# Performance work log

Measured on AMD Instinct MI355X. Metric: run time of the kernel, lower is better.

The kernel has to match this reference:

```python
import jax, jax.numpy as jnp
import numpy as np

N = 50000      # nodes
E = 800000     # edges (avg degree 16)
IN = 128       # input feature dim
HID = 32       # per-head hidden dim
H = 4          # attention heads
C = 40         # num classes
SLOPE = 0.2    # leaky relu negative slope


def setup_inputs() -> dict:
    key = jax.random.key(0)
    ks = jax.random.split(key, 14)
    s = 0.05
    inputs = jax.random.normal(ks[0], (N, IN), jnp.float32)
    target = jax.random.normal(ks[1], (N, IN), jnp.float32)
    lamb = jax.random.uniform(ks[2], (1,), jnp.float32)
    src = jax.random.randint(ks[3], (E,), 0, N, jnp.int32)
    dst = jax.random.randint(ks[4], (E,), 0, N, jnp.int32)
    W0 = jax.random.normal(ks[5], (IN, H * HID), jnp.float32) * s
    al0 = jax.random.normal(ks[6], (H, HID), jnp.float32) * s
    ar0 = jax.random.normal(ks[7], (H, HID), jnp.float32) * s
    W1 = jax.random.normal(ks[8], (H * HID, H * HID), jnp.float32) * s
    al1 = jax.random.normal(ks[9], (H, HID), jnp.float32) * s
    ar1 = jax.random.normal(ks[10], (H, HID), jnp.float32) * s
    Wout = jax.random.normal(ks[11], (H * HID, C), jnp.float32) * s
    bout = jnp.zeros((C,), jnp.float32)
    return dict(inputs=inputs, target=target, lamb=lamb,
                W0=W0, al0=al0, ar0=ar0, W1=W1, al1=al1, ar1=ar1,
                Wout=Wout, bout=bout, src=src, dst=dst)


def gat_conv(h, W, al, ar, src, dst, residual):
    # h: [N, in_dim]; W: [in_dim, H*HID]; al/ar: [H, HID]
    feat = (h @ W).reshape(N, H, HID)                  # [N,H,D]
    el = jnp.einsum('nhd,hd->nh', feat, al)            # [N,H]
    er = jnp.einsum('nhd,hd->nh', feat, ar)            # [N,H]
    e = jax.nn.leaky_relu(el[src] + er[dst], SLOPE)    # [E,H]
    # edge softmax over incoming edges of each dst node
    emax = jax.ops.segment_max(e, dst, num_segments=N)  # [N,H]
    ee = jnp.exp(e - emax[dst])                          # [E,H]
    denom = jax.ops.segment_sum(ee, dst, num_segments=N)
    a = ee / denom[dst]                                  # [E,H]
    msg = feat[src] * a[:, :, None]                      # [E,H,D]
    out = jax.ops.segment_sum(msg, dst, num_segments=N)  # [N,H,D]
    if residual:
        out = out + h.reshape(N, H, HID)  # identity residual (in == H*HID)
    return jax.nn.elu(out)


def reference(inputs, target, lamb, W0, al0, ar0, W1, al1, ar1, Wout, bout, src, dst):
    def path(x):
        h = gat_conv(x, W0, al0, ar0, src, dst, residual=False).reshape(N, H * HID)
        h = gat_conv(h, W1, al1, ar1, src, dst, residual=True).reshape(N, H * HID)
        return h

    h = path(inputs)
    h2 = path(target)
    lam = lamb[0]
    h = lam * h + (1.0 - lam) * h2   # mixup_hidden=True
    logits = h @ Wout + bout
    return (h, logits)
```

## Files before the change

### kernel.cpp

```cpp
#include <hip/hip_runtime.h>
#include <hip/hip_bf16.h>
#include <cstddef>

#define GN 50000
#define GE 800000
#define GH 4
#define GD 32
#define SLOPE 0.2f
#define LOG2E 1.4426950408889634f

typedef unsigned short ushort_t;
typedef unsigned int uint_t;
using short8 = __attribute__((ext_vector_type(8))) short;
using float4v = __attribute__((ext_vector_type(4))) float;

__device__ __forceinline__ ushort_t f2bf(float f) {
    union { float f; uint_t u; } v; v.f = f;
    uint_t r = v.u + 0x7fff + ((v.u >> 16) & 1);
    return (ushort_t)(r >> 16);
}
__device__ __forceinline__ float bflo(uint_t u) { return __uint_as_float(u << 16); }
__device__ __forceinline__ float bfhi(uint_t u) { return __uint_as_float(u & 0xffff0000u); }
__device__ __forceinline__ float bfu(ushort_t u) { return __uint_as_float((uint_t)u << 16); }

__device__ __forceinline__ uint_t cvt_pk_bf16(float lo, float hi) {
    uint_t r;
    asm("v_cvt_pk_bf16_f32 %0, %1, %2" : "=v"(r) : "v"(lo), "v"(hi));
    return r;
}

#if __has_builtin(__builtin_amdgcn_exp2f)
#define EXP2F(x) __builtin_amdgcn_exp2f(x)
#else
#define EXP2F(x) exp2f(x)
#endif

#define SWZ_B(v, imm) __uint_as_float((uint_t)__builtin_amdgcn_ds_swizzle((int)__float_as_uint(v), (imm)))

__global__ void k_hist(const int* __restrict__ dst, int* __restrict__ deg, int E) {
    int i = blockIdx.x * 256 + threadIdx.x;
    if (i < E) atomicAdd(&deg[dst[i]], 1);
}

__global__ void k_scan1(const int* __restrict__ deg, int* __restrict__ row_ptr,
                        int* __restrict__ partials, int n) {
    __shared__ int s[256];
    int t = threadIdx.x;
    int i = blockIdx.x * 256 + t;
    int v = (i < n) ? deg[i] : 0;
    s[t] = v;
    __syncthreads();
    for (int off = 1; off < 256; off <<= 1) {
        int add = (t >= off) ? s[t - off] : 0;
        __syncthreads();
        s[t] += add;
        __syncthreads();
    }
    if (i < n) row_ptr[i] = s[t] - v;
    if (t == 255) partials[blockIdx.x] = s[255];
}

__global__ void k_scan2(int* __restrict__ partials, int nb) {
    __shared__ int s[256];
    int t = threadIdx.x;
    int v = (t < nb) ? partials[t] : 0;
    s[t] = v;
    __syncthreads();
    for (int off = 1; off < 256; off <<= 1) {
        int add = (t >= off) ? s[t - off] : 0;
        __syncthreads();
        s[t] += add;
        __syncthreads();
    }
    if (t < nb) partials[t] = s[t] - v;
}

__global__ void k_scan3(int* __restrict__ row_ptr, int* __restrict__ wpos,
                        const int* __restrict__ partials, int n, int E) {
    int i = blockIdx.x * 256 + threadIdx.x;
    if (i < n) {
        int rp = row_ptr[i] + partials[i >> 8];
        row_ptr[i] = rp;
        wpos[i] = rp;
        if (i == 0) row_ptr[n] = E;
    }
}

__global__ void k_fill(const int* __restrict__ src, const int* __restrict__ dst,
                       int* __restrict__ wpos, int* __restrict__ csr_src, int E) {
    int i = blockIdx.x * 256 + threadIdx.x;
    if (i < E) {
        int p = atomicAdd(&wpos[dst[i]], 1);
        csr_src[p] = src[i];
    }
}

__global__ void k_cvt_w(const float* __restrict__ W0, const float* __restrict__ W1,
                        ushort_t* __restrict__ wbt) {
    int t = blockIdx.x * 256 + threadIdx.x;
    int m = t >> 14;
    int o = t & 16383;
    int n = o >> 7, k = o & 127;
    const float* W = m ? W1 : W0;
    wbt[t] = f2bf(W[k * 128 + n]);
}

__global__ void k_cvt_wout(const float* __restrict__ Wout, ushort_t* __restrict__ wb) {
    int t = blockIdx.x * 256 + threadIdx.x;
    if (t >= 48 * 128) return;
    int n = t >> 7, k = t & 127;
    float w = (n < 40) ? Wout[k * 40 + n] : 0.f;
    ushort_t h = f2bf(w);
    float r = w - bfu(h);
    wb[t] = h;
    wb[48 * 128 + t] = f2bf(r);
}

__device__ __forceinline__ void lr_epilogue(const float4v acc[2][8],
                                            const float* __restrict__ al,
                                            const float* __restrict__ ar,
                                            float* __restrict__ el,
                                            float* __restrict__ er,
                                            int r0, int quad, int col, int M) {
#pragma unroll
    for (int rt = 0; rt < 2; rt++) {
#pragma unroll
        for (int h = 0; h < 4; h++) {
            float alv0 = al[h * 32 + col], alv1 = al[h * 32 + 16 + col];
            float arv0 = ar[h * 32 + col], arv1 = ar[h * 32 + 16 + col];
            float pl[4], pr[4];
#pragma unroll
            for (int r = 0; r < 4; r++) {
                pl[r] = acc[rt][2 * h][r] * alv0 + acc[rt][2 * h + 1][r] * alv1;
                pr[r] = acc[rt][2 * h][r] * arv0 + acc[rt][2 * h + 1][r] * arv1;
            }
#pragma unroll
            for (int m = 1; m < 16; m <<= 1) {
#pragma unroll
                for (int r = 0; r < 4; r++) {
                    pl[r] += __shfl_xor(pl[r], m, 64);
                    pr[r] += __shfl_xor(pr[r], m, 64);
                }
            }
            if (col == h) {
#pragma unroll
                for (int r = 0; r < 4; r++) {
                    int row = r0 + rt * 16 + quad * 4 + r;
                    if (row < M) el[row * 4 + h] = pl[r] * LOG2E;
                }
            }
            if (col == 8 + h) {
#pragma unroll
                for (int r = 0; r < 4; r++) {
                    int row = r0 + rt * 16 + quad * 4 + r;
                    if (row < M) er[row * 4 + h] = pr[r] * LOG2E;
                }
            }
        }
    }
}

__device__ __forceinline__ void store_c_bf16(ushort_t* __restrict__ Cb,
                                             const float4v acc[2][8],
                                             int r0, int quad, int col, int M) {
#pragma unroll
    for (int rt = 0; rt < 2; rt++)
#pragma unroll
        for (int nt = 0; nt < 8; nt++) {
            int rb = r0 + rt * 16 + quad * 4;
            int c = nt * 16 + col;
            uint_t p01 = cvt_pk_bf16(acc[rt][nt][0], acc[rt][nt][1]);
            uint_t p23 = cvt_pk_bf16(acc[rt][nt][2], acc[rt][nt][3]);
            if (rb + 0 < M) Cb[(size_t)(rb + 0) * 128 + c] = (ushort_t)p01;
            if (rb + 1 < M) Cb[(size_t)(rb + 1) * 128 + c] = (ushort_t)(p01 >> 16);
            if (rb + 2 < M) Cb[(size_t)(rb + 2) * 128 + c] = (ushort_t)p23;
            if (rb + 3 < M) Cb[(size_t)(rb + 3) * 128 + c] = (ushort_t)(p23 >> 16);
        }
}

__global__ __launch_bounds__(256) void gemm_mfma32(const float* __restrict__ A0,
                                                   const float* __restrict__ A1,
                                                   const ushort_t* __restrict__ WbT,
                                                   const float* __restrict__ al,
                                                   const float* __restrict__ ar,
                                                   ushort_t* __restrict__ Cb,
                                                   float* __restrict__ el,
                                                   float* __restrict__ er, int M) {
    __shared__ ushort_t Bs[128][136];
    int tid = threadIdx.x;
    for (int i = tid; i < 128 * 16; i += 256) {
        int n = i >> 4;
        int kc = (i & 15) << 3;
        *(short8*)&Bs[n][kc] = *(const short8*)&WbT[n * 128 + kc];
    }
    __syncthreads();
    int wid = tid >> 6, lane = tid & 63;
    int r0 = blockIdx.x * 128 + wid * 32;
    int col = lane & 15, quad = lane >> 4;
    float4v acc[2][8];
#pragma unroll
    for (int rt = 0; rt < 2; rt++)
#pragma unroll
        for (int t = 0; t < 8; t++) acc[rt][t] = (float4v){0.f, 0.f, 0.f, 0.f};
    int ar_[2] = {r0 + col, r0 + 16 + col};
    const float* Ap[2];
#pragma unroll
    for (int rt = 0; rt < 2; rt++) {
        int a = ar_[rt];
        Ap[rt] = (a < M) ? ((a < GN) ? (A0 + (size_t)a * 128)
                                     : (A1 + (size_t)(a - GN) * 128)) : nullptr;
    }
#pragma unroll
    for (int ks = 0; ks < 4; ks++) {
        short8 af[2];
#pragma unroll
        for (int rt = 0; rt < 2; rt++) {
            af[rt] = (short8){};
            if (Ap[rt]) {
                float4 v0 = *(const float4*)&Ap[rt][ks * 32 + quad * 8];
                float4 v1 = *(const float4*)&Ap[rt][ks * 32 + quad * 8 + 4];
                union { short8 s; uint_t u[4]; } cv;
                cv.u[0] = cvt_pk_bf16(v0.x, v0.y);
                cv.u[1] = cvt_pk_bf16(v0.z, v0.w);
                cv.u[2] = cvt_pk_bf16(v1.x, v1.y);
                cv.u[3] = cvt_pk_bf16(v1.z, v1.w);
                af[rt] = cv.s;
            }
        }
#pragma unroll
        for (int nt = 0; nt < 8; nt++) {
            short8 bf = *(const short8*)&Bs[nt * 16 + col][ks * 32 + quad * 8];
            acc[0][nt] = __builtin_amdgcn_mfma_f32_16x16x32_bf16(af[0], bf, acc[0][nt], 0, 0, 0);
            acc[1][nt] = __builtin_amdgcn_mfma_f32_16x16x32_bf16(af[1], bf, acc[1][nt], 0, 0, 0);
        }
    }
    store_c_bf16(Cb, acc, r0, quad, col, M);
    lr_epilogue(acc, al, ar, el, er, r0, quad, col, M);
}

__global__ __launch_bounds__(256) void gemm_mfma(const ushort_t* __restrict__ A,
                                                 const ushort_t* __restrict__ WbT,
                                                 const float* __restrict__ al,
                                                 const float* __restrict__ ar,
                                                 ushort_t* __restrict__ Cb,
                                                 float* __restrict__ el,
                                                 float* __restrict__ er, int M) {
    __shared__ ushort_t Bs[128][136];
    int tid = threadIdx.x;
    for (int i = tid; i < 128 * 16; i += 256) {
        int n = i >> 4;
        int kc = (i & 15) << 3;
        *(short8*)&Bs[n][kc] = *(const short8*)&WbT[n * 128 + kc];
    }
    __syncthreads();
    int wid = tid >> 6, lane = tid & 63;
    int r0 = blockIdx.x * 128 + wid * 32;
    int col = lane & 15, quad = lane >> 4;
    float4v acc[2][8];
#pragma unroll
    for (int rt = 0; rt < 2; rt++)
#pragma unroll
        for (int t = 0; t < 8; t++) acc[rt][t] = (float4v){0.f, 0.f, 0.f, 0.f};
    int ar_[2] = {r0 + col, r0 + 16 + col};
#pragma unroll
    for (int ks = 0; ks < 4; ks++) {
        short8 af[2];
#pragma unroll
        for (int rt = 0; rt < 2; rt++) {
            af[rt] = (short8){};
            if (ar_[rt] < M) af[rt] = *(const short8*)&A[(size_t)ar_[rt] * 128 + ks * 32 + quad * 8];
        }
#pragma unroll
        for (int nt = 0; nt < 8; nt++) {
            short8 bf = *(const short8*)&Bs[nt * 16 + col][ks * 32 + quad * 8];
            acc[0][nt] = __builtin_amdgcn_mfma_f32_16x16x32_bf16(af[0], bf, acc[0][nt], 0, 0, 0);
            acc[1][nt] = __builtin_amdgcn_mfma_f32_16x16x32_bf16(af[1], bf, acc[1][nt], 0, 0, 0);
        }
    }
    store_c_bf16(Cb, acc, r0, quad, col, M);
    lr_epilogue(acc, al, ar, el, er, r0, quad, col, M);
}

__device__ __forceinline__ void agg_core(
    const ushort_t* __restrict__ featb, const float* __restrict__ el, float ern,
    const int* __restrict__ csr_src, int base, int deg, uint_t ebase, uint_t fofs,
    int lane, float& v0, float& v1, float& v2, float& v3) {
    float a0 = 0.f, a1 = 0.f, a2 = 0.f, a3 = 0.f, ss = 0.f;
    int nmain = deg & ~7;
    int lk = lane & 7;
    if (nmain) {
        int jb = base;
        int s0 = csr_src[jb + 0], s1 = csr_src[jb + 1], s2 = csr_src[jb + 2], s3 = csr_src[jb + 3];
        int s4 = csr_src[jb + 4], s5 = csr_src[jb + 5], s6 = csr_src[jb + 6], s7 = csr_src[jb + 7];
        int sown = csr_src[jb + lk];
        int i = 0;
        for (;;) {
            const ushort_t* p0 = featb + (uint_t)s0 * 128u;
            const ushort_t* p1 = featb + (uint_t)s1 * 128u;
            const ushort_t* p2 = featb + (uint_t)s2 * 128u;
            const ushort_t* p3 = featb + (uint_t)s3 * 128u;
            const ushort_t* p4 = featb + (uint_t)s4 * 128u;
            const ushort_t* p5 = featb + (uint_t)s5 * 128u;
            const ushort_t* p6 = featb + (uint_t)s6 * 128u;
            const ushort_t* p7 = featb + (uint_t)s7 * 128u;
            uint2 f0 = *(const uint2*)&p0[fofs];
            uint2 f1 = *(const uint2*)&p1[fofs];
            uint2 f2 = *(const uint2*)&p2[fofs];
            uint2 f3 = *(const uint2*)&p3[fofs];
            uint2 f4 = *(const uint2*)&p4[fofs];
            uint2 f5 = *(const uint2*)&p5[fofs];
            uint2 f6 = *(const uint2*)&p6[fofs];
            uint2 f7 = *(const uint2*)&p7[fofs];
            float e = el[ebase + (uint_t)sown * 4u] + ern;
            bool more = (i + 8) < nmain;
            int t0 = 0, t1 = 0, t2 = 0, t3 = 0, t4 = 0, t5 = 0, t6 = 0, t7 = 0, town = 0;
            if (more) {
                int nj = jb + 8;
                t0 = csr_src[nj + 0]; t1 = csr_src[nj + 1]; t2 = csr_src[nj + 2]; t3 = csr_src[nj + 3];
                t4 = csr_src[nj + 4]; t5 = csr_src[nj + 5]; t6 = csr_src[nj + 6]; t7 = csr_src[nj + 7];
                town = csr_src[nj + lk];
            }
            e = fmaxf(e, SLOPE * e);
            float wown = EXP2F(e);
            float w0 = SWZ_B(wown, 0x018);
            float w1 = SWZ_B(wown, 0x038);
            float w2 = SWZ_B(wown, 0x058);
            float w3 = SWZ_B(wown, 0x078);
            float w4 = SWZ_B(wown, 0x098);
            float w5 = SWZ_B(wown, 0x0B8);
            float w6 = SWZ_B(wown, 0x0D8);
            float w7 = SWZ_B(wown, 0x0F8);
            ss += ((w0 + w1) + (w2 + w3)) + ((w4 + w5) + (w6 + w7));
            a0 += w0 * bflo(f0.x) + w1 * bflo(f1.x) + w2 * bflo(f2.x) + w3 * bflo(f3.x) +
                  w4 * bflo(f4.x) + w5 * bflo(f5.x) + w6 * bflo(f6.x) + w7 * bflo(f7.x);
            a1 += w0 * bfhi(f0.x) + w1 * bfhi(f1.x) + w2 * bfhi(f2.x) + w3 * bfhi(f3.x) +
                  w4 * bfhi(f4.x) + w5 * bfhi(f5.x) + w6 * bfhi(f6.x) + w7 * bfhi(f7.x);
            a2 += w0 * bflo(f0.y) + w1 * bflo(f1.y) + w2 * bflo(f2.y) + w3 * bflo(f3.y) +
                  w4 * bflo(f4.y) + w5 * bflo(f5.y) + w6 * bflo(f6.y) + w7 * bflo(f7.y);
            a3 += w0 * bfhi(f0.y) + w1 * bfhi(f1.y) + w2 * bfhi(f2.y) + w3 * bfhi(f3.y) +
                  w4 * bfhi(f4.y) + w5 * bfhi(f5.y) + w6 * bfhi(f6.y) + w7 * bfhi(f7.y);
            if (!more) break;
            i += 8; jb += 8;
            s0 = t0; s1 = t1; s2 = t2; s3 = t3; s4 = t4; s5 = t5; s6 = t6; s7 = t7;
            sown = town;
        }
    }
    for (int i = nmain; i < deg; i++) {
        int s = csr_src[base + i];
        float e = el[ebase + (uint_t)s * 4u] + ern;
        const ushort_t* p = featb + (uint_t)s * 128u;
        uint2 f = *(const uint2*)&p[fofs];
        e = fmaxf(e, SLOPE * e);
        float w = EXP2F(e);
        ss += w;
        a0 += w * bflo(f.x);
        a1 += w * bfhi(f.x);
        a2 += w * bflo(f.y);
        a3 += w * bfhi(f.y);
    }
    float inv = (deg > 0) ? 1.f / ss : 0.f;
    v0 = a0 * inv; v1 = a1 * inv; v2 = a2 * inv; v3 = a3 * inv;
}

__global__ __launch_bounds__(256) void gat_agg_l1(
    const ushort_t* __restrict__ featb, const float* __restrict__ el,
    const float* __restrict__ er, const int* __restrict__ row_ptr,
    const int* __restrict__ csr_src, ushort_t* __restrict__ abuf) {
    int n = __builtin_amdgcn_readfirstlane(blockIdx.x * 4 + (threadIdx.x >> 6));
    if (n >= GN) return;
    int lane = threadIdx.x & 63;
    int half = lane >> 5;
    int q = lane & 31;
    int head = (lane >> 3) & 3, q4 = q << 2;
    uint_t ebase = (uint_t)(half * (GN * 4) + head);
    uint_t fofs = (uint_t)(half * (GN * 128) + q4);
    float ern = er[ebase + (uint_t)n * 4u];
    int base = row_ptr[n];
    int deg = row_ptr[n + 1] - base;
    float v0, v1, v2, v3;
    agg_core(featb, el, ern, csr_src, base, deg, ebase, fofs, lane, v0, v1, v2, v3);
    v0 = v0 > 0.f ? v0 : __expf(v0) - 1.f;
    v1 = v1 > 0.f ? v1 : __expf(v1) - 1.f;
    v2 = v2 > 0.f ? v2 : __expf(v2) - 1.f;
    v3 = v3 > 0.f ? v3 : __expf(v3) - 1.f;
    size_t idx = ((size_t)n + (size_t)half * GN) * 128 + q4;
    uint2 o;
    o.x = cvt_pk_bf16(v0, v1);
    o.y = cvt_pk_bf16(v2, v3);
    *(uint2*)&abuf[idx] = o;
}

__global__ __launch_bounds__(256) void gat_agg_l2(
    const ushort_t* __restrict__ featb, const float* __restrict__ el,
    const float* __restrict__ er, const int* __restrict__ row_ptr,
    const int* __restrict__ csr_src, const ushort_t* __restrict__ resid,
    const float* __restrict__ lamb, float* __restrict__ outh) {
    int tid = threadIdx.x;
    int n = __builtin_amdgcn_readfirstlane(blockIdx.x * 4 + (tid >> 6));
    if (n >= GN) return;
    int lane = tid & 63;
    int half = lane >> 5;
    int q = lane & 31;
    int head = (lane >> 3) & 3, q4 = q << 2;
    uint_t ebase = (uint_t)(half * (GN * 4) + head);
    uint_t fofs = (uint_t)(half * (GN * 128) + q4);
    float ern = er[ebase + (uint_t)n * 4u];
    int base = row_ptr[n];
    int deg = row_ptr[n + 1] - base;
    float v0, v1, v2, v3;
    agg_core(featb, el, ern, csr_src, base, deg, ebase, fofs, lane, v0, v1, v2, v3);
    size_t idx = ((size_t)n + (size_t)half * GN) * 128 + q4;
    ushort4 r = *(const ushort4*)&resid[idx];
    v0 += bfu(r.x); v1 += bfu(r.y); v2 += bfu(r.z); v3 += bfu(r.w);
    v0 = v0 > 0.f ? v0 : __expf(v0) - 1.f;
    v1 = v1 > 0.f ? v1 : __expf(v1) - 1.f;
    v2 = v2 > 0.f ? v2 : __expf(v2) - 1.f;
    v3 = v3 > 0.f ? v3 : __expf(v3) - 1.f;
    float p0 = __shfl_xor(v0, 32, 64);
    float p1 = __shfl_xor(v1, 32, 64);
    float p2 = __shfl_xor(v2, 32, 64);
    float p3 = __shfl_xor(v3, 32, 64);
    float lam = lamb[0];
    if (half == 0) {
        float m0 = lam * v0 + (1.f - lam) * p0;
        float m1 = lam * v1 + (1.f - lam) * p1;
        float m2 = lam * v2 + (1.f - lam) * p2;
        float m3 = lam * v3 + (1.f - lam) * p3;
        *(float4*)&outh[(size_t)n * 128 + q4] = make_float4(m0, m1, m2, m3);
    }
}

__global__ __launch_bounds__(256) void k_logits(const float* __restrict__ Hf,
                                                const ushort_t* __restrict__ Wb,
                                                const float* __restrict__ bout,
                                                float* __restrict__ outlog) {
    __shared__ ushort_t Bh[48][136];
    __shared__ ushort_t Bl[48][136];
    int tid = threadIdx.x;
    for (int i = tid; i < 48 * 16; i += 256) {
        int n = i >> 4;
        int kc = (i & 15) << 3;
        *(short8*)&Bh[n][kc] = *(const short8*)&Wb[n * 128 + kc];
        *(short8*)&Bl[n][kc] = *(const short8*)&Wb[48 * 128 + n * 128 + kc];
    }
    __syncthreads();
    int wid = tid >> 6, lane = tid & 63;
    int r0 = blockIdx.x * 128 + wid * 32;
    int col = lane & 15, quad = lane >> 4;
    float4v acc[2][3];
#pragma unroll
    for (int rt = 0; rt < 2; rt++)
#pragma unroll
        for (int nt = 0; nt < 3; nt++) acc[rt][nt] = (float4v){0.f, 0.f, 0.f, 0.f};
    int ar_[2] = {r0 + col, r0 + 16 + col};
#pragma unroll
    for (int ks = 0; ks < 4; ks++) {
        short8 ah[2], alo[2];
#pragma unroll
        for (int rt = 0; rt < 2; rt++) {
            ah[rt] = (short8){};
            alo[rt] = (short8){};
            if (ar_[rt] < GN) {
                const float* p = Hf + (size_t)ar_[rt] * 128 + ks * 32 + quad * 8;
                float4 x = *(const float4*)p;
                float4 y = *(const float4*)(p + 4);
                union { short8 s; uint_t u[4]; } ch, cl;
                ch.u[0] = cvt_pk_bf16(x.x, x.y);
                ch.u[1] = cvt_pk_bf16(x.z, x.w);
                ch.u[2] = cvt_pk_bf16(y.x, y.y);
                ch.u[3] = cvt_pk_bf16(y.z, y.w);
                cl.u[0] = cvt_pk_bf16(x.x - bflo(ch.u[0]), x.y - bfhi(ch.u[0]));
                cl.u[1] = cvt_pk_bf16(x.z - bflo(ch.u[1]), x.w - bfhi(ch.u[1]));
                cl.u[2] = cvt_pk_bf16(y.x - bflo(ch.u[2]), y.y - bfhi(ch.u[2]));
                cl.u[3] = cvt_pk_bf16(y.z - bflo(ch.u[3]), y.w - bfhi(ch.u[3]));
                ah[rt] = ch.s;
                alo[rt] = cl.s;
            }
        }
#pragma unroll
        for (int nt = 0; nt < 3; nt++) {
            short8 bh = *(const short8*)&Bh[nt * 16 + col][ks * 32 + quad * 8];
            short8 bl = *(const short8*)&Bl[nt * 16 + col][ks * 32 + quad * 8];
#pragma unroll
            for (int rt = 0; rt < 2; rt++) {
                acc[rt][nt] = __builtin_amdgcn_mfma_f32_16x16x32_bf16(ah[rt], bh, acc[rt][nt], 0, 0, 0);
                acc[rt][nt] = __builtin_amdgcn_mfma_f32_16x16x32_bf16(alo[rt], bh, acc[rt][nt], 0, 0, 0);
                acc[rt][nt] = __builtin_amdgcn_mfma_f32_16x16x32_bf16(ah[rt], bl, acc[rt][nt], 0, 0, 0);
            }
        }
    }
#pragma unroll
    for (int nt = 0; nt < 3; nt++) {
        int c = nt * 16 + col;
        if (c < 40) {
            float bv = bout[c];
#pragma unroll
            for (int rt = 0; rt < 2; rt++)
#pragma unroll
                for (int r = 0; r < 4; r++) {
                    int row = r0 + rt * 16 + quad * 4 + r;
                    if (row < GN) outlog[(size_t)row * 40 + c] = acc[rt][nt][r] + bv;
                }
        }
    }
}

extern "C" void kernel_launch(void* const* d_in, const int* in_sizes, int n_in,
                              void* d_out, int out_size, void* d_ws, size_t ws_size,
                              hipStream_t stream) {
    const float* inputs = (const float*)d_in[0];
    const float* target = (const float*)d_in[1];
    const float* lamb   = (const float*)d_in[2];
    const float* W0     = (const float*)d_in[3];
    const float* al0    = (const float*)d_in[4];
    const float* ar0    = (const float*)d_in[5];
    const float* W1     = (const float*)d_in[6];
    const float* al1    = (const float*)d_in[7];
    const float* ar1    = (const float*)d_in[8];
    const float* Wout   = (const float*)d_in[9];
    const float* bout   = (const float*)d_in[10];
    const int*   src    = (const int*)d_in[11];
    const int*   dst    = (const int*)d_in[12];

    float* out = (float*)d_out;
    float* outh = out;
    float* outlog = out + (size_t)GN * 128;

    const int NP = 2 * GN;
    ushort_t* featb = (ushort_t*)d_ws;
    ushort_t* abuf  = featb + (size_t)NP * 128;
    float* el = (float*)(abuf + (size_t)NP * 128);
    float* er = el + (size_t)NP * GH;
    ushort_t* wbt = (ushort_t*)(er + (size_t)NP * GH);
    int* row_ptr  = (int*)(wbt + 2 * 128 * 128);
    int* wpos     = row_ptr + (GN + 1);
    int* csr_src  = wpos + GN;
    int* partials = csr_src + GE + 16;
    ushort_t* woutb = (ushort_t*)(partials + 256);

    const int nb = (GN + 255) / 256;
    const int eb = (GE + 255) / 256;
    const int gblocks = (NP + 127) / 128;
    const int aggblocks = (GN + 3) / 4;
    const int lblocks = (GN + 127) / 128;

    hipMemsetAsync(wpos, 0, GN * sizeof(int), stream);
    k_hist<<<eb, 256, 0, stream>>>(dst, wpos, GE);
    k_scan1<<<nb, 256, 0, stream>>>(wpos, row_ptr, partials, GN);
    k_scan2<<<1, 256, 0, stream>>>(partials, nb);
    k_scan3<<<nb, 256, 0, stream>>>(row_ptr, wpos, partials, GN, GE);
    k_fill<<<eb, 256, 0, stream>>>(src, dst, wpos, csr_src, GE);

    k_cvt_w<<<128, 256, 0, stream>>>(W0, W1, wbt);
    k_cvt_wout<<<24, 256, 0, stream>>>(Wout, woutb);

    gemm_mfma32<<<gblocks, 256, 0, stream>>>(inputs, target, wbt, al0, ar0,
                                             featb, el, er, NP);
    gat_agg_l1<<<aggblocks, 256, 0, stream>>>(featb, el, er, row_ptr, csr_src, abuf);

    gemm_mfma<<<gblocks, 256, 0, stream>>>(abuf, wbt + 128 * 128, al1, ar1,
                                           featb, el, er, NP);
    gat_agg_l2<<<aggblocks, 256, 0, stream>>>(featb, el, er, row_ptr, csr_src,
                                              abuf, lamb, outh);

    k_logits<<<lblocks, 256, 0, stream>>>(outh, woutb, bout, outlog);
}
```

Before: 415.2 us.

## Interleave input/target node rows and unify edge loop with masked tail

```diff
diff --git a/kernel.cpp b/kernel.cpp
--- a/kernel.cpp
+++ b/kernel.cpp
@@ -36,6 +36,10 @@
 #endif
 
 #define SWZ_B(v, imm) __uint_as_float((uint_t)__builtin_amdgcn_ds_swizzle((int)__float_as_uint(v), (imm)))
+
+__device__ __forceinline__ int slotmap(int a) {
+    return (a < GN) ? (a << 1) : (((a - GN) << 1) | 1);
+}
 
 __global__ void k_hist(const int* __restrict__ dst, int* __restrict__ deg, int E) {
     int i = blockIdx.x * 256 + threadIdx.x;
@@ -146,14 +150,14 @@
 #pragma unroll
                 for (int r = 0; r < 4; r++) {
                     int row = r0 + rt * 16 + quad * 4 + r;
-                    if (row < M) el[row * 4 + h] = pl[r] * LOG2E;
+                    if (row < M) el[slotmap(row) * 4 + h] = pl[r] * LOG2E;
                 }
             }
             if (col == 8 + h) {
 #pragma unroll
                 for (int r = 0; r < 4; r++) {
                     int row = r0 + rt * 16 + quad * 4 + r;
-                    if (row < M) er[row * 4 + h] = pr[r] * LOG2E;
+                    if (row < M) er[slotmap(row) * 4 + h] = pr[r] * LOG2E;
                 }
             }
         }
@@ -171,10 +175,10 @@
             int c = nt * 16 + col;
             uint_t p01 = cvt_pk_bf16(acc[rt][nt][0], acc[rt][nt][1]);
             uint_t p23 = cvt_pk_bf16(acc[rt][nt][2], acc[rt][nt][3]);
-            if (rb + 0 < M) Cb[(size_t)(rb + 0) * 128 + c] = (ushort_t)p01;
-            if (rb + 1 < M) Cb[(size_t)(rb + 1) * 128 + c] = (ushort_t)(p01 >> 16);
-            if (rb + 2 < M) Cb[(size_t)(rb + 2) * 128 + c] = (ushort_t)p23;
-            if (rb + 3 < M) Cb[(size_t)(rb + 3) * 128 + c] = (ushort_t)(p23 >> 16);
+            if (rb + 0 < M) Cb[(size_t)slotmap(rb + 0) * 128 + c] = (ushort_t)p01;
+            if (rb + 1 < M) Cb[(size_t)slotmap(rb + 1) * 128 + c] = (ushort_t)(p01 >> 16);
+            if (rb + 2 < M) Cb[(size_t)slotmap(rb + 2) * 128 + c] = (ushort_t)p23;
+            if (rb + 3 < M) Cb[(size_t)slotmap(rb + 3) * 128 + c] = (ushort_t)(p23 >> 16);
         }
 }
 
@@ -262,13 +266,19 @@
 #pragma unroll
         for (int t = 0; t < 8; t++) acc[rt][t] = (float4v){0.f, 0.f, 0.f, 0.f};
     int ar_[2] = {r0 + col, r0 + 16 + col};
+    const ushort_t* Ap[2];
+#pragma unroll
+    for (int rt = 0; rt < 2; rt++) {
+        int a = ar_[rt];
+        Ap[rt] = (a < M) ? (A + (size_t)slotmap(a) * 128) : nullptr;
+    }
 #pragma unroll
     for (int ks = 0; ks < 4; ks++) {
         short8 af[2];
 #pragma unroll
         for (int rt = 0; rt < 2; rt++) {
             af[rt] = (short8){};
-            if (ar_[rt] < M) af[rt] = *(const short8*)&A[(size_t)ar_[rt] * 128 + ks * 32 + quad * 8];
+            if (Ap[rt]) af[rt] = *(const short8*)&Ap[rt][ks * 32 + quad * 8];
         }
 #pragma unroll
         for (int nt = 0; nt < 8; nt++) {
@@ -285,96 +295,100 @@
     const ushort_t* __restrict__ featb, const float* __restrict__ el, float ern,
     const int* __restrict__ csr_src, int base, int deg, uint_t ebase, uint_t fofs,
     int lane, float& v0, float& v1, float& v2, float& v3) {
+    if (deg <= 0) { v0 = v1 = v2 = v3 = 0.f; return; }
     float a0 = 0.f, a1 = 0.f, a2 = 0.f, a3 = 0.f, ss = 0.f;
-    int nmain = deg & ~7;
     int lk = lane & 7;
-    if (nmain) {
-        int jb = base;
-        int s0 = csr_src[jb + 0], s1 = csr_src[jb + 1], s2 = csr_src[jb + 2], s3 = csr_src[jb + 3];
-        int s4 = csr_src[jb + 4], s5 = csr_src[jb + 5], s6 = csr_src[jb + 6], s7 = csr_src[jb + 7];
-        int sown = csr_src[jb + lk];
-        int i = 0;
-        for (;;) {
-            const ushort_t* p0 = featb + (uint_t)s0 * 128u;
-            const ushort_t* p1 = featb + (uint_t)s1 * 128u;
-            const ushort_t* p2 = featb + (uint_t)s2 * 128u;
-            const ushort_t* p3 = featb + (uint_t)s3 * 128u;
-            const ushort_t* p4 = featb + (uint_t)s4 * 128u;
-            const ushort_t* p5 = featb + (uint_t)s5 * 128u;
-            const ushort_t* p6 = featb + (uint_t)s6 * 128u;
-            const ushort_t* p7 = featb + (uint_t)s7 * 128u;
-            uint2 f0 = *(const uint2*)&p0[fofs];
-            uint2 f1 = *(const uint2*)&p1[fofs];
-            uint2 f2 = *(const uint2*)&p2[fofs];
-            uint2 f3 = *(const uint2*)&p3[fofs];
-            uint2 f4 = *(const uint2*)&p4[fofs];
-            uint2 f5 = *(const uint2*)&p5[fofs];
-            uint2 f6 = *(const uint2*)&p6[fofs];
-            uint2 f7 = *(const uint2*)&p7[fofs];
-            float e = el[ebase + (uint_t)sown * 4u] + ern;
-            bool more = (i + 8) < nmain;
-            int t0 = 0, t1 = 0, t2 = 0, t3 = 0, t4 = 0, t5 = 0, t6 = 0, t7 = 0, town = 0;
-            if (more) {
-                int nj = jb + 8;
-                t0 = csr_src[nj + 0]; t1 = csr_src[nj + 1]; t2 = csr_src[nj + 2]; t3 = csr_src[nj + 3];
-                t4 = csr_src[nj + 4]; t5 = csr_src[nj + 5]; t6 = csr_src[nj + 6]; t7 = csr_src[nj + 7];
-                town = csr_src[nj + lk];
-            }
-            e = fmaxf(e, SLOPE * e);
-            float wown = EXP2F(e);
-            float w0 = SWZ_B(wown, 0x018);
-            float w1 = SWZ_B(wown, 0x038);
-            float w2 = SWZ_B(wown, 0x058);
-            float w3 = SWZ_B(wown, 0x078);
-            float w4 = SWZ_B(wown, 0x098);
-            float w5 = SWZ_B(wown, 0x0B8);
-            float w6 = SWZ_B(wown, 0x0D8);
-            float w7 = SWZ_B(wown, 0x0F8);
-            ss += ((w0 + w1) + (w2 + w3)) + ((w4 + w5) + (w6 + w7));
-            a0 += w0 * bflo(f0.x) + w1 * bflo(f1.x) + w2 * bflo(f2.x) + w3 * bflo(f3.x) +
-                  w4 * bflo(f4.x) + w5 * bflo(f5.x) + w6 * bflo(f6.x) + w7 * bflo(f7.x);
-            a1 += w0 * bfhi(f0.x) + w1 * bfhi(f1.x) + w2 * bfhi(f2.x) + w3 * bfhi(f3.x) +
-                  w4 * bfhi(f4.x) + w5 * bfhi(f5.x) + w6 * bfhi(f6.x) + w7 * bfhi(f7.x);
-            a2 += w0 * bflo(f0.y) + w1 * bflo(f1.y) + w2 * bflo(f2.y) + w3 * bflo(f3.y) +
-                  w4 * bflo(f4.y) + w5 * bflo(f5.y) + w6 * bflo(f6.y) + w7 * bflo(f7.y);
-            a3 += w0 * bfhi(f0.y) + w1 * bfhi(f1.y) + w2 * bfhi(f2.y) + w3 * bfhi(f3.y) +
-                  w4 * bfhi(f4.y) + w5 * bfhi(f5.y) + w6 * bfhi(f6.y) + w7 * bfhi(f7.y);
-            if (!more) break;
-            i += 8; jb += 8;
-            s0 = t0; s1 = t1; s2 = t2; s3 = t3; s4 = t4; s5 = t5; s6 = t6; s7 = t7;
-            sown = town;
-        }
-    }
-    for (int i = nmain; i < deg; i++) {
-        int s = csr_src[base + i];
-        float e = el[ebase + (uint_t)s * 4u] + ern;
-        const ushort_t* p = featb + (uint_t)s * 128u;
-        uint2 f = *(const uint2*)&p[fofs];
+    int nblk = (deg + 7) >> 3;
+    int jb = base;
+    int r1 = deg - 1;
+    int s0 = csr_src[jb];
+    int s1 = csr_src[jb + min(1, r1)];
+    int s2 = csr_src[jb + min(2, r1)];
+    int s3 = csr_src[jb + min(3, r1)];
+    int s4 = csr_src[jb + min(4, r1)];
+    int s5 = csr_src[jb + min(5, r1)];
+    int s6 = csr_src[jb + min(6, r1)];
+    int s7 = csr_src[jb + min(7, r1)];
+    int sown = csr_src[jb + min(lk, r1)];
+    float eown = el[ebase + (uint_t)sown * 8u];
+    int b = 0;
+    for (;;) {
+        int rem = deg - (b << 3);
+        const ushort_t* p0 = featb + (uint_t)s0 * 256u;
+        const ushort_t* p1 = featb + (uint_t)s1 * 256u;
+        const ushort_t* p2 = featb + (uint_t)s2 * 256u;
+        const ushort_t* p3 = featb + (uint_t)s3 * 256u;
+        const ushort_t* p4 = featb + (uint_t)s4 * 256u;
+        const ushort_t* p5 = featb + (uint_t)s5 * 256u;
+        const ushort_t* p6 = featb + (uint_t)s6 * 256u;
+        const ushort_t* p7 = featb + (uint_t)s7 * 256u;
+        uint2 f0 = *(const uint2*)&p0[fofs];
+        uint2 f1 = *(const uint2*)&p1[fofs];
+        uint2 f2 = *(const uint2*)&p2[fofs];
+        uint2 f3 = *(const uint2*)&p3[fofs];
+        uint2 f4 = *(const uint2*)&p4[fofs];
+        uint2 f5 = *(const uint2*)&p5[fofs];
+        uint2 f6 = *(const uint2*)&p6[fofs];
+        uint2 f7 = *(const uint2*)&p7[fofs];
+        bool more = (b + 1) < nblk;
+        int t0 = 0, t1 = 0, t2 = 0, t3 = 0, t4 = 0, t5 = 0, t6 = 0, t7 = 0, town = 0;
+        float eon = 0.f;
+        if (more) {
+            int nj = jb + 8;
+            int r2 = rem - 9;
+            t0 = csr_src[nj];
+            t1 = csr_src[nj + min(1, r2)];
+            t2 = csr_src[nj + min(2, r2)];
+            t3 = csr_src[nj + min(3, r2)];
+            t4 = csr_src[nj + min(4, r2)];
+            t5 = csr_src[nj + min(5, r2)];
+            t6 = csr_src[nj + min(6, r2)];
+            t7 = csr_src[nj + min(7, r2)];
+            town = csr_src[nj + min(lk, r2)];
+            eon = el[ebase + (uint_t)town * 8u];
+        }
+        float e = (lk < rem) ? (eown + ern) : -1e38f;
         e = fmaxf(e, SLOPE * e);
-        float w = EXP2F(e);
-        ss += w;
-        a0 += w * bflo(f.x);
-        a1 += w * bfhi(f.x);
-        a2 += w * bflo(f.y);
-        a3 += w * bfhi(f.y);
-    }
-    float inv = (deg > 0) ? 1.f / ss : 0.f;
+        float wown = EXP2F(e);
+        float w0 = SWZ_B(wown, 0x018);
+        float w1 = SWZ_B(wown, 0x038);
+        float w2 = SWZ_B(wown, 0x058);
+        float w3 = SWZ_B(wown, 0x078);
+        float w4 = SWZ_B(wown, 0x098);
+        float w5 = SWZ_B(wown, 0x0B8);
+        float w6 = SWZ_B(wown, 0x0D8);
+        float w7 = SWZ_B(wown, 0x0F8);
+        ss += ((w0 + w1) + (w2 + w3)) + ((w4 + w5) + (w6 + w7));
+        a0 += w0 * bflo(f0.x) + w1 * bflo(f1.x) + w2 * bflo(f2.x) + w3 * bflo(f3.x) +
+              w4 * bflo(f4.x) + w5 * bflo(f5.x) + w6 * bflo(f6.x) + w7 * bflo(f7.x);
+        a1 += w0 * bfhi(f0.x) + w1 * bfhi(f1.x) + w2 * bfhi(f2.x) + w3 * bfhi(f3.x) +
+              w4 * bfhi(f4.x) + w5 * bfhi(f5.x) + w6 * bfhi(f6.x) + w7 * bfhi(f7.x);
+        a2 += w0 * bflo(f0.y) + w1 * bflo(f1.y) + w2 * bflo(f2.y) + w3 * bflo(f3.y) +
+              w4 * bflo(f4.y) + w5 * bflo(f5.y) + w6 * bflo(f6.y) + w7 * bflo(f7.y);
+        a3 += w0 * bfhi(f0.y) + w1 * bfhi(f1.y) + w2 * bfhi(f2.y) + w3 * bfhi(f3.y) +
+              w4 * bfhi(f4.y) + w5 * bfhi(f5.y) + w6 * bfhi(f6.y) + w7 * bfhi(f7.y);
+        if (!more) break;
+        b++; jb += 8;
+        s0 = t0; s1 = t1; s2 = t2; s3 = t3; s4 = t4; s5 = t5; s6 = t6; s7 = t7;
+        sown = town; eown = eon;
+    }
+    float inv = 1.f / ss;
     v0 = a0 * inv; v1 = a1 * inv; v2 = a2 * inv; v3 = a3 * inv;
 }
 
-__global__ __launch_bounds__(256) void gat_agg_l1(
+__global__ __launch_bounds__(512) void gat_agg_l1(
     const ushort_t* __restrict__ featb, const float* __restrict__ el,
     const float* __restrict__ er, const int* __restrict__ row_ptr,
     const int* __restrict__ csr_src, ushort_t* __restrict__ abuf) {
-    int n = __builtin_amdgcn_readfirstlane(blockIdx.x * 4 + (threadIdx.x >> 6));
+    int n = __builtin_amdgcn_readfirstlane(blockIdx.x * 8 + (threadIdx.x >> 6));
     if (n >= GN) return;
     int lane = threadIdx.x & 63;
     int half = lane >> 5;
     int q = lane & 31;
     int head = (lane >> 3) & 3, q4 = q << 2;
-    uint_t ebase = (uint_t)(half * (GN * 4) + head);
-    uint_t fofs = (uint_t)(half * (GN * 128) + q4);
-    float ern = er[ebase + (uint_t)n * 4u];
+    uint_t ebase = (uint_t)(half * 4 + head);
+    uint_t fofs = (uint_t)(half * 128 + q4);
+    float ern = er[(uint_t)n * 8u + ebase];
     int base = row_ptr[n];
     int deg = row_ptr[n + 1] - base;
     float v0, v1, v2, v3;
@@ -383,33 +397,33 @@
     v1 = v1 > 0.f ? v1 : __expf(v1) - 1.f;
     v2 = v2 > 0.f ? v2 : __expf(v2) - 1.f;
     v3 = v3 > 0.f ? v3 : __expf(v3) - 1.f;
-    size_t idx = ((size_t)n + (size_t)half * GN) * 128 + q4;
+    size_t idx = ((size_t)(2 * n + half)) * 128 + q4;
     uint2 o;
     o.x = cvt_pk_bf16(v0, v1);
     o.y = cvt_pk_bf16(v2, v3);
     *(uint2*)&abuf[idx] = o;
 }
 
-__global__ __launch_bounds__(256) void gat_agg_l2(
+__global__ __launch_bounds__(512) void gat_agg_l2(
     const ushort_t* __restrict__ featb, const float* __restrict__ el,
     const float* __restrict__ er, const int* __restrict__ row_ptr,
     const int* __restrict__ csr_src, const ushort_t* __restrict__ resid,
     const float* __restrict__ lamb, float* __restrict__ outh) {
     int tid = threadIdx.x;
-    int n = __builtin_amdgcn_readfirstlane(blockIdx.x * 4 + (tid >> 6));
+    int n = __builtin_amdgcn_readfirstlane(blockIdx.x * 8 + (tid >> 6));
     if (n >= GN) return;
     int lane = tid & 63;
     int half = lane >> 5;
     int q = lane & 31;
     int head = (lane >> 3) & 3, q4 = q << 2;
-    uint_t ebase = (uint_t)(half * (GN * 4) + head);
-    uint_t fofs = (uint_t)(half * (GN * 128) + q4);
-    float ern = er[ebase + (uint_t)n * 4u];
+    uint_t ebase = (uint_t)(half * 4 + head);
+    uint_t fofs = (uint_t)(half * 128 + q4);
+    float ern = er[(uint_t)n * 8u + ebase];
     int base = row_ptr[n];
     int deg = row_ptr[n + 1] - base;
     float v0, v1, v2, v3;
     agg_core(featb, el, ern, csr_src, base, deg, ebase, fofs, lane, v0, v1, v2, v3);
-    size_t idx = ((size_t)n + (size_t)half * GN) * 128 + q4;
+    size_t idx = ((size_t)(2 * n + half)) * 128 + q4;
     ushort4 r = *(const ushort4*)&resid[idx];
     v0 += bfu(r.x); v1 += bfu(r.y); v2 += bfu(r.z); v3 += bfu(r.w);
     v0 = v0 > 0.f ? v0 : __expf(v0) - 1.f;
@@ -541,7 +555,7 @@
     const int nb = (GN + 255) / 256;
     const int eb = (GE + 255) / 256;
     const int gblocks = (NP + 127) / 128;
-    const int aggblocks = (GN + 3) / 4;
+    const int aggblocks = (GN + 7) / 8;
     const int lblocks = (GN + 127) / 128;
 
     hipMemsetAsync(wpos, 0, GN * sizeof(int), stream);
@@ -556,11 +570,11 @@
 
     gemm_mfma32<<<gblocks, 256, 0, stream>>>(inputs, target, wbt, al0, ar0,
                                              featb, el, er, NP);
-    gat_agg_l1<<<aggblocks, 256, 0, stream>>>(featb, el, er, row_ptr, csr_src, abuf);
+    gat_agg_l1<<<aggblocks, 512, 0, stream>>>(featb, el, er, row_ptr, csr_src, abuf);
 
     gemm_mfma<<<gblocks, 256, 0, stream>>>(abuf, wbt + 128 * 128, al1, ar1,
                                            featb, el, er, NP);
-    gat_agg_l2<<<aggblocks, 256, 0, stream>>>(featb, el, er, row_ptr, csr_src,
+    gat_agg_l2<<<aggblocks, 512, 0, stream>>>(featb, el, er, row_ptr, csr_src,
                                               abuf, lamb, outh);
 
     k_logits<<<lblocks, 256, 0, stream>>>(outh, woutb, bout, outlog);
```

Result: faster. 406.8 us (-2.0%).
